# Optimization experiments

Hardware: AMD Instinct MI355X
Metric: run time of the kernel (lower is better)

The kernel has to match this reference:

```python
import jax, jax.numpy as jnp
import numpy as np

NUM_SEGMENTS = 1024  # number of distinct group ids in ix (fill_max)
DIM = 384


def setup_inputs() -> dict:
    key = jax.random.key(0)
    ks = jax.random.split(key, 8)
    H = 65536
    x = jax.random.normal(ks[0], (1, H, DIM), dtype=jnp.float32)
    ix = jax.random.randint(ks[1], (1, H), 0, NUM_SEGMENTS, dtype=jnp.int64)
    s = 0.05  # keep g(x) in a numerically tame range before exp
    f_w = jax.random.normal(ks[2], (DIM, DIM), dtype=jnp.float32) * s
    f_b = jax.random.normal(ks[3], (DIM,), dtype=jnp.float32) * s
    g_w = jax.random.normal(ks[4], (DIM, DIM), dtype=jnp.float32) * s
    g_b = jax.random.normal(ks[5], (DIM,), dtype=jnp.float32) * s
    h_w = jax.random.normal(ks[6], (DIM, DIM), dtype=jnp.float32) * s
    h_b = jax.random.normal(ks[7], (DIM,), dtype=jnp.float32) * s
    return {"x": x, "ix": ix, "f_w": f_w, "f_b": f_b, "g_w": g_w,
            "g_b": g_b, "h_w": h_w, "h_b": h_b}


def reference(x, ix, f_w, f_b, g_w, g_b, h_w, h_b):
    # x: [1, H, C]; ix: [1, H] group ids. Original builds an [H,H] equality
    # mask; the math is exactly a per-group softmax(g(x))-weighted sum of f(x)
    # broadcast back to every member of the group, so we use segment_sum.
    ix0 = ix[0]                                   # [H]
    fx = x[0] @ f_w.T + f_b                       # [H, C]
    gx = jnp.clip(x[0] @ g_w.T + g_b, -50.0, 50.0)
    w = jnp.exp(gx)                               # [H, C]
    denom = jax.ops.segment_sum(w, ix0, num_segments=NUM_SEGMENTS)  # [S, C]
    denom = jnp.maximum(denom, 1e-9)
    wi = w / denom[ix0]                           # normalized weights, [H, C]
    num = jax.ops.segment_sum(fx * wi, ix0, num_segments=NUM_SEGMENTS)  # [S, C]
    y = num[ix0][None]                            # [1, H, C]
    return y @ h_w.T + h_b
```

## Files before the change

### kernel.cpp

```cpp
#include <hip/hip_runtime.h>

#define DIM 384
#define NSEG 1024
#define CHUNK 64
#define LDA 392
#define MAXLS 16

typedef __attribute__((ext_vector_type(8))) short bf16x8;
typedef __attribute__((ext_vector_type(4))) float f32x4;

static __device__ __forceinline__ short f2bf(float f) {
    union { float f; unsigned u; } v{f};
    unsigned r = (v.u + 0x7FFFu + ((v.u >> 16) & 1u)) >> 16;
    return (short)r;
}

#define PACK_BLOCKS ((2 * 24 * 12 * 64) / 256)

__global__ void prep_kernel(const int* __restrict__ ix, int* __restrict__ hist,
                            const float* __restrict__ fw, const float* __restrict__ gw,
                            short* __restrict__ pb, int H) {
    int b = blockIdx.x;
    if (b < PACK_BLOCKS) {
        int idx = b * 256 + threadIdx.x;
        int lane = idx & 63;
        int ks   = (idx >> 6) % 12;
        int T    = ((idx >> 6) / 12) % 24;
        int mat  = idx / (64 * 12 * 24);
        const float* src = mat ? gw : fw;
        int ch = T * 16 + (lane & 15);
        int k0 = ks * 32 + (lane >> 4) * 8;
        short* dst = pb + (size_t)idx * 8;
#pragma unroll
        for (int e = 0; e < 8; e++) dst[e] = f2bf(src[(size_t)ch * DIM + k0 + e]);
    } else {
        int i = (b - PACK_BLOCKS) * 256 + threadIdx.x;
        if (i < H) atomicAdd(&hist[ix[i]], 1);
    }
}


__global__ void scan_kernel(const int* __restrict__ hist, int* __restrict__ seg_start,
                            int* __restrict__ cursor) {
    __shared__ int tmp[NSEG];
    int t = threadIdx.x;
    int v = hist[t];
    tmp[t] = v;
    __syncthreads();
    for (int off = 1; off < NSEG; off <<= 1) {
        int add = (t >= off) ? tmp[t - off] : 0;
        __syncthreads();
        tmp[t] += add;
        __syncthreads();
    }
    int incl = tmp[t];
    seg_start[t] = incl - v;
    cursor[t]    = incl - v;
    if (t == NSEG - 1) seg_start[NSEG] = incl;
}

__global__ void scatter_kernel(const int* __restrict__ ix, int* __restrict__ cursor,
                               int* __restrict__ order, int H) {
    int i = blockIdx.x * blockDim.x + threadIdx.x;
    if (i < H) {
        int p = atomicAdd(&cursor[ix[i]], 1);
        order[p] = i;
    }
}

__global__ __launch_bounds__(512, 3) void seg_gemm_chunk(
    const float* __restrict__ x, const short* __restrict__ pb,
    const float* __restrict__ f_b, const float* __restrict__ g_b,
    const int* __restrict__ order, const int* __restrict__ ix,
    float* __restrict__ den_acc, float* __restrict__ num_acc) {
    const int chunk0 = blockIdx.x * CHUNK;
    const int tid  = threadIdx.x;
    const int lane = tid & 63;
    const int wave = tid >> 6;
    const int n    = lane & 15;
    const int q    = lane >> 4;
    const int cb   = wave * 48;

    __shared__ short As[CHUNK * LDA];
    __shared__ int   segrow[CHUNK];

    {
        int r  = tid >> 3;
        int c8 = tid & 7;
        int gr = order[chunk0 + r];
        if (c8 == 0) segrow[r] = ix[gr];
        const f32x4* xr = (const f32x4*)(x + (size_t)gr * DIM);
        short* dst = &As[r * LDA];
#pragma unroll
        for (int i = 0; i < 12; i++) {
            f32x4 v = __builtin_nontemporal_load(xr + c8 + 8 * i);
            short4 s = { f2bf(v[0]), f2bf(v[1]), f2bf(v[2]), f2bf(v[3]) };
            *(short4*)&dst[(c8 + 8 * i) * 4] = s;
        }
    }
    __syncthreads();

    float fbv[3], gbv[3];
#pragma unroll
    for (int t = 0; t < 3; t++) {
        fbv[t] = f_b[cb + t * 16 + n];
        gbv[t] = g_b[cb + t * 16 + n];
    }

    f32x4 accf[4][3], accg[4][3];
#pragma unroll
    for (int rt = 0; rt < 4; rt++)
#pragma unroll
        for (int t = 0; t < 3; t++) {
            accf[rt][t] = (f32x4){0.f, 0.f, 0.f, 0.f};
            accg[rt][t] = (f32x4){0.f, 0.f, 0.f, 0.f};
        }

#pragma unroll
    for (int ks = 0; ks < 12; ks++) {
        bf16x8 a[4];
#pragma unroll
        for (int rt = 0; rt < 4; rt++)
            a[rt] = *(const bf16x8*)&As[(rt * 16 + n) * LDA + ks * 32 + q * 8];
#pragma unroll
        for (int t = 0; t < 3; t++) {
            int Tg = wave * 3 + t;
            bf16x8 bfr = *(const bf16x8*)(pb + ((size_t)((0 * 24 + Tg) * 12 + ks)) * 512 + lane * 8);
            bf16x8 bgr = *(const bf16x8*)(pb + ((size_t)((1 * 24 + Tg) * 12 + ks)) * 512 + lane * 8);
#pragma unroll
            for (int rt = 0; rt < 4; rt++) {
                accf[rt][t] = __builtin_amdgcn_mfma_f32_16x16x32_bf16(a[rt], bfr, accf[rt][t], 0, 0, 0);
                accg[rt][t] = __builtin_amdgcn_mfma_f32_16x16x32_bf16(a[rt], bgr, accg[rt][t], 0, 0, 0);
            }
        }
    }

    const int s0 = segrow[0];
    __syncthreads();
    float* accs = (float*)As;
    for (int i = tid; i < MAXLS * DIM * 2; i += 512) accs[i] = 0.f;
    __syncthreads();

#pragma unroll
    for (int t = 0; t < 3; t++) {
        int ch = cb + t * 16 + n;
        float rw = 0.f, rf = 0.f;
        int cur = -1;
#pragma unroll
        for (int rt = 0; rt < 4; rt++) {
#pragma unroll
            for (int r = 0; r < 4; r++) {
                int m  = rt * 16 + q * 4 + r;
                int ls = segrow[m] - s0;
                if (ls != cur) {
                    if (cur >= 0) {
                        if (cur < MAXLS) {
                            atomicAdd(&accs[(cur * DIM + ch) * 2 + 0], rw);
                            atomicAdd(&accs[(cur * DIM + ch) * 2 + 1], rf);
                        } else {
                            atomicAdd(&den_acc[(size_t)(s0 + cur) * DIM + ch], rw);
                            atomicAdd(&num_acc[(size_t)(s0 + cur) * DIM + ch], rf);
                        }
                    }
                    cur = ls; rw = 0.f; rf = 0.f;
                }
                float gx = accg[rt][t][r] + gbv[t];
                gx = fmaxf(-50.f, fminf(50.f, gx));
                float w = __expf(gx);
                rw += w;
                rf += (accf[rt][t][r] + fbv[t]) * w;
            }
        }
        if (cur < MAXLS) {
            atomicAdd(&accs[(cur * DIM + ch) * 2 + 0], rw);
            atomicAdd(&accs[(cur * DIM + ch) * 2 + 1], rf);
        } else {
            atomicAdd(&den_acc[(size_t)(s0 + cur) * DIM + ch], rw);
            atomicAdd(&num_acc[(size_t)(s0 + cur) * DIM + ch], rf);
        }
    }
    __syncthreads();

    int nls = segrow[CHUNK - 1] - s0 + 1;
    if (nls > MAXLS) nls = MAXLS;
    for (int i = tid; i < nls * DIM; i += 512) {
        int ls = i / DIM, ch = i - ls * DIM;
        float dw = accs[(ls * DIM + ch) * 2 + 0];
        float dn = accs[(ls * DIM + ch) * 2 + 1];
        if (dw != 0.f || dn != 0.f) {
            atomicAdd(&den_acc[(size_t)(s0 + ls) * DIM + ch], dw);
            atomicAdd(&num_acc[(size_t)(s0 + ls) * DIM + ch], dn);
        }
    }
}

__global__ __launch_bounds__(256) void hgemm_kernel(
    const float* __restrict__ num, const float* __restrict__ den,
    const float* __restrict__ h_w, const float* __restrict__ h_b,
    float* __restrict__ z) {
    const int m0 = blockIdx.x * 64;
    const int c0 = blockIdx.y * 64;
    const int tid = threadIdx.x;
    const int ty = tid >> 4, tx = tid & 15;
    __shared__ float As[16][64];
    __shared__ float Bs[16][64];
    float acc[4][4];
#pragma unroll
    for (int i = 0; i < 4; i++)
#pragma unroll
        for (int j = 0; j < 4; j++) acc[i][j] = 0.f;

    for (int k0 = 0; k0 < DIM; k0 += 16) {
        __syncthreads();
        {
            int m  = tid >> 2;
            int kq = (tid & 3) << 2;
            size_t idx = (size_t)(m0 + m) * DIM + k0 + kq;
            float4 v = *(const float4*)(num + idx);
            float4 d = *(const float4*)(den + idx);
            v.x /= fmaxf(d.x, 1e-9f); v.y /= fmaxf(d.y, 1e-9f);
            v.z /= fmaxf(d.z, 1e-9f); v.w /= fmaxf(d.w, 1e-9f);
            As[kq + 0][m] = v.x; As[kq + 1][m] = v.y;
            As[kq + 2][m] = v.z; As[kq + 3][m] = v.w;
            float4 w = *(const float4*)(h_w + (size_t)(c0 + m) * DIM + k0 + kq);
            Bs[kq + 0][m] = w.x; Bs[kq + 1][m] = w.y;
            Bs[kq + 2][m] = w.z; Bs[kq + 3][m] = w.w;
        }
        __syncthreads();
#pragma unroll
        for (int kk = 0; kk < 16; kk++) {
            float a[4], b[4];
#pragma unroll
            for (int i = 0; i < 4; i++) a[i] = As[kk][ty * 4 + i];
#pragma unroll
            for (int j = 0; j < 4; j++) b[j] = Bs[kk][tx * 4 + j];
#pragma unroll
            for (int i = 0; i < 4; i++)
#pragma unroll
                for (int j = 0; j < 4; j++) acc[i][j] += a[i] * b[j];
        }
    }
#pragma unroll
    for (int i = 0; i < 4; i++)
#pragma unroll
        for (int j = 0; j < 4; j++)
            z[(size_t)(m0 + ty * 4 + i) * DIM + c0 + tx * 4 + j] = acc[i][j] + h_b[c0 + tx * 4 + j];
}

__global__ void gather_kernel(const int* __restrict__ ix, const f32x4* __restrict__ z,
                              f32x4* __restrict__ out, int H) {
    int t = blockIdx.x * blockDim.x + threadIdx.x;
    int total = H * (DIM / 4);
    if (t < total) {
        int i = t / (DIM / 4);
        int qq = t - i * (DIM / 4);
        f32x4 v = z[(size_t)ix[i] * (DIM / 4) + qq];
        __builtin_nontemporal_store(v, out + (size_t)i * (DIM / 4) + qq);
    }
}

extern "C" void kernel_launch(void* const* d_in, const int* in_sizes, int n_in,
                              void* d_out, int out_size, void* d_ws, size_t ws_size,
                              hipStream_t stream) {
    const float* x   = (const float*)d_in[0];
    const int*   ix  = (const int*)d_in[1];
    const float* f_w = (const float*)d_in[2];
    const float* f_b = (const float*)d_in[3];
    const float* g_w = (const float*)d_in[4];
    const float* g_b = (const float*)d_in[5];
    const float* h_w = (const float*)d_in[6];
    const float* h_b = (const float*)d_in[7];
    float* out = (float*)d_out;
    const int H = in_sizes[0] / DIM;

    char* w = (char*)d_ws;
    int* hist      = (int*)w;   w += 4096;
    int* seg_start = (int*)w;   w += 8192;
    int* cursor    = (int*)w;   w += 4096;
    int* order     = (int*)w;   w += (size_t)H * 4;
    float* den_acc = (float*)w; w += (size_t)NSEG * DIM * 4;
    float* num_acc = (float*)w; w += (size_t)NSEG * DIM * 4;
    float* z       = (float*)w; w += (size_t)NSEG * DIM * 4;
    short* pb      = (short*)w;

    (void)hipMemsetAsync(hist, 0, NSEG * sizeof(int), stream);
    (void)hipMemsetAsync(den_acc, 0, (size_t)2 * NSEG * DIM * 4, stream);
    prep_kernel<<<PACK_BLOCKS + (H + 255) / 256, 256, 0, stream>>>(ix, hist, f_w, g_w, pb, H);
    scan_kernel<<<1, NSEG, 0, stream>>>(hist, seg_start, cursor);
    scatter_kernel<<<(H + 255) / 256, 256, 0, stream>>>(ix, cursor, order, H);
    seg_gemm_chunk<<<H / CHUNK, 512, 0, stream>>>(x, pb, f_b, g_b, order, ix,
                                                  den_acc, num_acc);
    hgemm_kernel<<<dim3(NSEG / 64, DIM / 64), 256, 0, stream>>>(num_acc, den_acc,
                                                                h_w, h_b, z);
    gather_kernel<<<(H * (DIM / 4) + 255) / 256, 256, 0, stream>>>(
        ix, (const f32x4*)z, (f32x4*)out, H);
}
```

Before: 334.2 us.

## Split f/g GEMM across wave groups, process multiple chunks per block with prefetch

Restructures the segmented GEMM kernel into 1024-thread blocks: waves 0-7 compute the f projection and waves 8-15 the g projection. The g waves write exp weights to shared memory for the f waves, and each block walks four chunks, prefetching the next chunk's x rows while the current epilogue runs. The shared-memory per-segment staging is removed, so partial sums go straight to global atomics, and the hgemm inner loop reads float4 from shared memory. This lowers register pressure per wave and hides load latency, at the cost of more global atomics and extra barriers per chunk.

```diff
diff --git a/kernel.cpp b/kernel.cpp
--- a/kernel.cpp
+++ b/kernel.cpp
@@ -4,7 +4,8 @@
 #define NSEG 1024
 #define CHUNK 64
 #define LDA 392
-#define MAXLS 16
+#define WPAD 50
+#define CPB 4
 
 typedef __attribute__((ext_vector_type(8))) short bf16x8;
 typedef __attribute__((ext_vector_type(4))) float f32x4;
@@ -68,129 +69,160 @@
     }
 }
 
-__global__ __launch_bounds__(512, 3) void seg_gemm_chunk(
+__global__ __launch_bounds__(1024, 4) void seg_gemm_chunk(
     const float* __restrict__ x, const short* __restrict__ pb,
     const float* __restrict__ f_b, const float* __restrict__ g_b,
     const int* __restrict__ order, const int* __restrict__ ix,
-    float* __restrict__ den_acc, float* __restrict__ num_acc) {
-    const int chunk0 = blockIdx.x * CHUNK;
+    float* __restrict__ den_acc, float* __restrict__ num_acc, int nchunks) {
+
+    __shared__ char uni[8 * CHUNK * WPAD * 4];
+    __shared__ int segrow[2][CHUNK];
+    __shared__ int norder[CHUNK];
+
+    short* As = (short*)uni;
+    float* W  = (float*)uni;
+
     const int tid  = threadIdx.x;
     const int lane = tid & 63;
     const int wave = tid >> 6;
-    const int n    = lane & 15;
-    const int q    = lane >> 4;
-    const int cb   = wave * 48;
-
-    __shared__ short As[CHUNK * LDA];
-    __shared__ int   segrow[CHUNK];
+    const int n = lane & 15, q = lane >> 4;
+    const bool isG = wave >= 8;
+    const int pair = isG ? wave - 8 : wave;
+    const int cb   = pair * 48;
+
+    const int gc0 = blockIdx.x * CPB;
+    int mych = nchunks - gc0;
+    if (mych <= 0) return;
+    if (mych > CPB) mych = CPB;
+
+    float bv[3];
+#pragma unroll
+    for (int t = 0; t < 3; t++)
+        bv[t] = (isG ? g_b : f_b)[cb + t * 16 + n];
+
+    const int r  = tid >> 4;
+    const int c6 = tid & 15;
 
     {
-        int r  = tid >> 3;
-        int c8 = tid & 7;
-        int gr = order[chunk0 + r];
-        if (c8 == 0) segrow[r] = ix[gr];
+        int gr = order[gc0 * CHUNK + r];
+        if (c6 == 0) segrow[0][r] = ix[gr];
         const f32x4* xr = (const f32x4*)(x + (size_t)gr * DIM);
+        f32x4 sv[6];
+#pragma unroll
+        for (int i = 0; i < 6; i++) sv[i] = __builtin_nontemporal_load(xr + c6 + 16 * i);
         short* dst = &As[r * LDA];
 #pragma unroll
-        for (int i = 0; i < 12; i++) {
-            f32x4 v = __builtin_nontemporal_load(xr + c8 + 8 * i);
-            short4 s = { f2bf(v[0]), f2bf(v[1]), f2bf(v[2]), f2bf(v[3]) };
-            *(short4*)&dst[(c8 + 8 * i) * 4] = s;
+        for (int i = 0; i < 6; i++) {
+            short4 s = { f2bf(sv[i][0]), f2bf(sv[i][1]), f2bf(sv[i][2]), f2bf(sv[i][3]) };
+            *(short4*)&dst[(c6 + 16 * i) * 4] = s;
         }
     }
     __syncthreads();
 
-    float fbv[3], gbv[3];
-#pragma unroll
-    for (int t = 0; t < 3; t++) {
-        fbv[t] = f_b[cb + t * 16 + n];
-        gbv[t] = g_b[cb + t * 16 + n];
-    }
-
-    f32x4 accf[4][3], accg[4][3];
-#pragma unroll
-    for (int rt = 0; rt < 4; rt++)
-#pragma unroll
-        for (int t = 0; t < 3; t++) {
-            accf[rt][t] = (f32x4){0.f, 0.f, 0.f, 0.f};
-            accg[rt][t] = (f32x4){0.f, 0.f, 0.f, 0.f};
-        }
-
-#pragma unroll
-    for (int ks = 0; ks < 12; ks++) {
-        bf16x8 a[4];
+    for (int c = 0; c < mych; c++) {
+        const int buf = c & 1;
+        const bool hn = (c + 1) < mych;
+
+        int nxt_gr = 0;
+        if (wave == 8 && hn) nxt_gr = order[(gc0 + c + 1) * CHUNK + lane];
+
+        f32x4 acc[4][3];
 #pragma unroll
         for (int rt = 0; rt < 4; rt++)
-            a[rt] = *(const bf16x8*)&As[(rt * 16 + n) * LDA + ks * 32 + q * 8];
-#pragma unroll
-        for (int t = 0; t < 3; t++) {
-            int Tg = wave * 3 + t;
-            bf16x8 bfr = *(const bf16x8*)(pb + ((size_t)((0 * 24 + Tg) * 12 + ks)) * 512 + lane * 8);
-            bf16x8 bgr = *(const bf16x8*)(pb + ((size_t)((1 * 24 + Tg) * 12 + ks)) * 512 + lane * 8);
-#pragma unroll
-            for (int rt = 0; rt < 4; rt++) {
-                accf[rt][t] = __builtin_amdgcn_mfma_f32_16x16x32_bf16(a[rt], bfr, accf[rt][t], 0, 0, 0);
-                accg[rt][t] = __builtin_amdgcn_mfma_f32_16x16x32_bf16(a[rt], bgr, accg[rt][t], 0, 0, 0);
+#pragma unroll
+            for (int t = 0; t < 3; t++) acc[rt][t] = (f32x4){0.f, 0.f, 0.f, 0.f};
+
+        const size_t mb = isG ? 24 : 0;
+#pragma unroll
+        for (int ks = 0; ks < 12; ks++) {
+            bf16x8 a[4];
+#pragma unroll
+            for (int rt = 0; rt < 4; rt++)
+                a[rt] = *(const bf16x8*)&As[(rt * 16 + n) * LDA + ks * 32 + q * 8];
+#pragma unroll
+            for (int t = 0; t < 3; t++) {
+                bf16x8 bf = *(const bf16x8*)(pb + ((mb + pair * 3 + t) * 12 + ks) * 512 + lane * 8);
+#pragma unroll
+                for (int rt = 0; rt < 4; rt++)
+                    acc[rt][t] = __builtin_amdgcn_mfma_f32_16x16x32_bf16(a[rt], bf, acc[rt][t], 0, 0, 0);
             }
         }
-    }
-
-    const int s0 = segrow[0];
-    __syncthreads();
-    float* accs = (float*)As;
-    for (int i = tid; i < MAXLS * DIM * 2; i += 512) accs[i] = 0.f;
-    __syncthreads();
-
-#pragma unroll
-    for (int t = 0; t < 3; t++) {
-        int ch = cb + t * 16 + n;
-        float rw = 0.f, rf = 0.f;
-        int cur = -1;
-#pragma unroll
-        for (int rt = 0; rt < 4; rt++) {
-#pragma unroll
-            for (int r = 0; r < 4; r++) {
-                int m  = rt * 16 + q * 4 + r;
-                int ls = segrow[m] - s0;
-                if (ls != cur) {
-                    if (cur >= 0) {
-                        if (cur < MAXLS) {
-                            atomicAdd(&accs[(cur * DIM + ch) * 2 + 0], rw);
-                            atomicAdd(&accs[(cur * DIM + ch) * 2 + 1], rf);
-                        } else {
-                            atomicAdd(&den_acc[(size_t)(s0 + cur) * DIM + ch], rw);
-                            atomicAdd(&num_acc[(size_t)(s0 + cur) * DIM + ch], rf);
+        __syncthreads();
+
+        int nseg = 0;
+        if (wave == 8 && hn) {
+            nseg = ix[nxt_gr];
+            norder[lane] = nxt_gr;
+        }
+
+        if (isG) {
+#pragma unroll
+            for (int t = 0; t < 3; t++) {
+                int ch = cb + t * 16 + n;
+                float rw = 0.f; int cur = -1;
+#pragma unroll
+                for (int rt = 0; rt < 4; rt++)
+#pragma unroll
+                    for (int rr = 0; rr < 4; rr++) {
+                        int m = rt * 16 + q * 4 + rr;
+                        int seg = segrow[buf][m];
+                        float gx = acc[rt][t][rr] + bv[t];
+                        gx = fmaxf(-50.f, fminf(50.f, gx));
+                        float w = __expf(gx);
+                        W[((size_t)pair * CHUNK + m) * WPAD + t * 16 + n] = w;
+                        if (seg != cur) {
+                            if (cur >= 0) atomicAdd(&den_acc[(size_t)cur * DIM + ch], rw);
+                            cur = seg; rw = 0.f;
                         }
+                        rw += w;
                     }
-                    cur = ls; rw = 0.f; rf = 0.f;
-                }
-                float gx = accg[rt][t][r] + gbv[t];
-                gx = fmaxf(-50.f, fminf(50.f, gx));
-                float w = __expf(gx);
-                rw += w;
-                rf += (accf[rt][t][r] + fbv[t]) * w;
+                atomicAdd(&den_acc[(size_t)cur * DIM + ch], rw);
             }
         }
-        if (cur < MAXLS) {
-            atomicAdd(&accs[(cur * DIM + ch) * 2 + 0], rw);
-            atomicAdd(&accs[(cur * DIM + ch) * 2 + 1], rf);
-        } else {
-            atomicAdd(&den_acc[(size_t)(s0 + cur) * DIM + ch], rw);
-            atomicAdd(&num_acc[(size_t)(s0 + cur) * DIM + ch], rf);
-        }
-    }
-    __syncthreads();
-
-    int nls = segrow[CHUNK - 1] - s0 + 1;
-    if (nls > MAXLS) nls = MAXLS;
-    for (int i = tid; i < nls * DIM; i += 512) {
-        int ls = i / DIM, ch = i - ls * DIM;
-        float dw = accs[(ls * DIM + ch) * 2 + 0];
-        float dn = accs[(ls * DIM + ch) * 2 + 1];
-        if (dw != 0.f || dn != 0.f) {
-            atomicAdd(&den_acc[(size_t)(s0 + ls) * DIM + ch], dw);
-            atomicAdd(&num_acc[(size_t)(s0 + ls) * DIM + ch], dn);
-        }
+        __syncthreads();
+
+        f32x4 sv[6];
+        if (hn) {
+            int grn = norder[r];
+            const f32x4* xr = (const f32x4*)(x + (size_t)grn * DIM);
+#pragma unroll
+            for (int i = 0; i < 6; i++) sv[i] = __builtin_nontemporal_load(xr + c6 + 16 * i);
+        }
+
+        if (!isG) {
+#pragma unroll
+            for (int t = 0; t < 3; t++) {
+                int ch = cb + t * 16 + n;
+                float rf = 0.f; int cur = -1;
+#pragma unroll
+                for (int rt = 0; rt < 4; rt++)
+#pragma unroll
+                    for (int rr = 0; rr < 4; rr++) {
+                        int m = rt * 16 + q * 4 + rr;
+                        int seg = segrow[buf][m];
+                        float w = W[((size_t)pair * CHUNK + m) * WPAD + t * 16 + n];
+                        float val = (acc[rt][t][rr] + bv[t]) * w;
+                        if (seg != cur) {
+                            if (cur >= 0) atomicAdd(&num_acc[(size_t)cur * DIM + ch], rf);
+                            cur = seg; rf = 0.f;
+                        }
+                        rf += val;
+                    }
+                atomicAdd(&num_acc[(size_t)cur * DIM + ch], rf);
+            }
+        }
+        if (wave == 8 && hn) segrow[buf ^ 1][lane] = nseg;
+        __syncthreads();
+
+        if (hn) {
+            short* dst = &As[r * LDA];
+#pragma unroll
+            for (int i = 0; i < 6; i++) {
+                short4 s = { f2bf(sv[i][0]), f2bf(sv[i][1]), f2bf(sv[i][2]), f2bf(sv[i][3]) };
+                *(short4*)&dst[(c6 + 16 * i) * 4] = s;
+            }
+        }
+        __syncthreads();
     }
 }
 
@@ -229,11 +261,10 @@
         __syncthreads();
 #pragma unroll
         for (int kk = 0; kk < 16; kk++) {
-            float a[4], b[4];
-#pragma unroll
-            for (int i = 0; i < 4; i++) a[i] = As[kk][ty * 4 + i];
-#pragma unroll
-            for (int j = 0; j < 4; j++) b[j] = Bs[kk][tx * 4 + j];
+            float4 a4 = *(const float4*)&As[kk][ty * 4];
+            float4 b4 = *(const float4*)&Bs[kk][tx * 4];
+            float a[4] = { a4.x, a4.y, a4.z, a4.w };
+            float b[4] = { b4.x, b4.y, b4.z, b4.w };
 #pragma unroll
             for (int i = 0; i < 4; i++)
 #pragma unroll
@@ -272,6 +303,7 @@
     const float* h_b = (const float*)d_in[7];
     float* out = (float*)d_out;
     const int H = in_sizes[0] / DIM;
+    const int nchunks = H / CHUNK;
 
     char* w = (char*)d_ws;
     int* hist      = (int*)w;   w += 4096;
@@ -288,8 +320,8 @@
     prep_kernel<<<PACK_BLOCKS + (H + 255) / 256, 256, 0, stream>>>(ix, hist, f_w, g_w, pb, H);
     scan_kernel<<<1, NSEG, 0, stream>>>(hist, seg_start, cursor);
     scatter_kernel<<<(H + 255) / 256, 256, 0, stream>>>(ix, cursor, order, H);
-    seg_gemm_chunk<<<H / CHUNK, 512, 0, stream>>>(x, pb, f_b, g_b, order, ix,
-                                                  den_acc, num_acc);
+    seg_gemm_chunk<<<(nchunks + CPB - 1) / CPB, 1024, 0, stream>>>(
+        x, pb, f_b, g_b, order, ix, den_acc, num_acc, nchunks);
     hgemm_kernel<<<dim3(NSEG / 64, DIM / 64), 256, 0, stream>>>(num_acc, den_acc,
                                                                 h_w, h_b, z);
     gather_kernel<<<(H * (DIM / 4) + 255) / 256, 256, 0, stream>>>(
```

After: 457.1 us. 1.37x slower.
